# Performance work log

Hardware: AMD Instinct MI355X
Metric: run time of the kernel (lower is better)

The kernel has to match this reference:

```python
import jax, jax.numpy as jnp
import numpy as np

POS_FREQ = 6
DIR_FREQ = 4
HIDDEN = 128
N = 1048576


def pos_encode(x, num_freq):
    # x: (..., D) -> (..., D * 2 * num_freq); per-dim layout [sin(f0..fL-1), cos(f0..fL-1)]
    freqs = 2.0 ** jnp.arange(num_freq, dtype=x.dtype)
    xf = x[..., None] * freqs * jnp.pi  # (..., D, L)
    enc = jnp.concatenate([jnp.sin(xf), jnp.cos(xf)], axis=-1)  # (..., D, 2L)
    return enc.reshape(*x.shape[:-1], x.shape[-1] * 2 * num_freq)


def _linear_params(key, fan_in, fan_out):
    kw, kb = jax.random.split(key)
    bound = 1.0 / np.sqrt(fan_in)
    w = jax.random.uniform(kw, (fan_in, fan_out), jnp.float32, -bound, bound)
    b = jax.random.uniform(kb, (fan_out,), jnp.float32, -bound, bound)
    return w, b


def setup_inputs() -> dict:
    key = jax.random.key(0)
    ks = jax.random.split(key, 12)
    pos_in = 3 * 2 * POS_FREQ   # 36
    dir_in = 3 * 2 * DIR_FREQ   # 24
    positions = jax.random.uniform(ks[0], (N, 3), jnp.float32)
    directions = jax.random.normal(ks[1], (N, 3), jnp.float32)
    directions = directions / jnp.linalg.norm(directions, axis=-1, keepdims=True)
    g1_w, g1_b = _linear_params(ks[2], pos_in, HIDDEN)
    g2_w, g2_b = _linear_params(ks[3], HIDDEN, HIDDEN)
    g3_w, g3_b = _linear_params(ks[4], HIDDEN, HIDDEN)
    g4_w, g4_b = _linear_params(ks[5], HIDDEN, HIDDEN)
    d_w, d_b = _linear_params(ks[6], HIDDEN, 1)
    f_w, f_b = _linear_params(ks[7], HIDDEN, HIDDEN)
    c1_w, c1_b = _linear_params(ks[8], HIDDEN + dir_in, HIDDEN // 2)
    c2_w, c2_b = _linear_params(ks[9], HIDDEN // 2, 3)
    return {
        "positions": positions, "directions": directions,
        "g1_w": g1_w, "g1_b": g1_b, "g2_w": g2_w, "g2_b": g2_b,
        "g3_w": g3_w, "g3_b": g3_b, "g4_w": g4_w, "g4_b": g4_b,
        "d_w": d_w, "d_b": d_b, "f_w": f_w, "f_b": f_b,
        "c1_w": c1_w, "c1_b": c1_b, "c2_w": c2_w, "c2_b": c2_b,
    }


def reference(positions, directions,
              g1_w, g1_b, g2_w, g2_b, g3_w, g3_b, g4_w, g4_b,
              d_w, d_b, f_w, f_b, c1_w, c1_b, c2_w, c2_b):
    pos_enc = pos_encode(positions, POS_FREQ)   # (N, 36)
    dir_enc = pos_encode(directions, DIR_FREQ)  # (N, 24)
    h = jax.nn.relu(pos_enc @ g1_w + g1_b)
    h = jax.nn.relu(h @ g2_w + g2_b)
    h = jax.nn.relu(h @ g3_w + g3_b)
    geo_feat = jax.nn.relu(h @ g4_w + g4_b)     # (N, 128)
    density = jax.nn.softplus(geo_feat @ d_w + d_b)  # (N, 1)
    feature = geo_feat @ f_w + f_b              # (N, 128)
    color_in = jnp.concatenate([feature, dir_enc], axis=-1)  # (N, 152)
    c = jax.nn.relu(color_in @ c1_w + c1_b)
    rgb = jax.nn.sigmoid(c @ c2_w + c2_b)       # (N, 3)
    return rgb, density.squeeze(-1)
```

## Files before the change

kernel.cpp:

```cpp
#include <hip/hip_runtime.h>


typedef _Float16 half8 __attribute__((ext_vector_type(8)));
typedef _Float16 half2v __attribute__((ext_vector_type(2)));
typedef float f32x4 __attribute__((ext_vector_type(4)));

typedef __attribute__((address_space(1))) const unsigned int GU32;
typedef __attribute__((address_space(3))) unsigned int LU32;

#define MFMA16(A,B,C) __builtin_amdgcn_mfma_f32_16x16x32_f16(A,B,C,0,0,0)

#define G1A 0
#define G1B 4096
#define G2A 8192
#define G2B 16384
#define G3A 24576
#define G3B 32768
#define G4A 40960
#define G4B 49152
#define DCH 57344
#define FAC 59392
#define FBC 67584
#define C1C 75776
#define C2C 88064
#define IMG_HALVES 90112

__device__ __forceinline__ int permk(int s){
  int ks = s >> 5, gg = (s >> 3) & 3, jj = s & 7;
  return (2*ks + (jj >> 2))*16 + gg*4 + (jj & 3);
}

__global__ void prep(const float* __restrict__ g1w, const float* __restrict__ g2w,
                     const float* __restrict__ g3w, const float* __restrict__ g4w,
                     const float* __restrict__ dw,  const float* __restrict__ fw,
                     const float* __restrict__ c1w, const float* __restrict__ c2w,
                     _Float16* __restrict__ img) {
  int i = blockIdx.x*256 + threadIdx.x;
  if (i >= IMG_HALVES) return;
  float v; int o_loc, s, krowb, cb;
  if (i < G2A) {
    cb = (i < G1B) ? G1A : G1B; int obase = (i < G1B) ? 0 : 64;
    int r = i - cb; o_loc = r >> 6; s = r & 63; krowb = 128;
    v = (s < 36) ? g1w[s*128 + obase + o_loc] : 0.f;
  } else if (i < DCH) {
    int r = i - G2A; int ch = r >> 13;
    cb = G2A + ch*8192; int li = r & 8191;
    const float* W = (ch < 2) ? g2w : (ch < 4) ? g3w : g4w;
    int obase = (ch & 1)*64;
    o_loc = li >> 7; s = li & 127; krowb = 256;
    v = W[permk(s)*128 + obase + o_loc];
  } else if (i < FAC) {
    cb = DCH; int r = i - DCH; o_loc = r >> 7; s = r & 127; krowb = 256;
    v = (o_loc == 0) ? dw[permk(s)] : 0.f;
  } else if (i < C1C) {
    cb = (i < FBC) ? FAC : FBC; int obase = (i < FBC) ? 0 : 64;
    int r = i - cb; o_loc = r >> 7; s = r & 127; krowb = 256;
    v = fw[permk(s)*128 + obase + o_loc];
  } else if (i < C2C) {
    cb = C1C; int r = i - C1C; o_loc = r/192; s = r%192; krowb = 384;
    v = (s < 128) ? c1w[permk(s)*64 + o_loc]
      : (s < 152) ? c1w[s*64 + o_loc] : 0.f;
  } else {
    cb = C2C; int r = i - C2C; o_loc = r >> 7; s = r & 127; krowb = 256;
    v = (s < 64 && o_loc < 3) ? c2w[permk(s)*3 + o_loc] : 0.f;
  }
  int byte_in = (o_loc*krowb + 2*s) ^ ((o_loc & 7) << 4);
  *(_Float16*)((char*)img + (size_t)cb*2 + byte_in) = (_Float16)v;
}

__device__ __forceinline__ half8 mk8(uint2 a, uint2 b){
  union { unsigned int u[4]; half8 h; } x;
  x.u[0]=a.x; x.u[1]=a.y; x.u[2]=b.x; x.u[3]=b.y; return x.h;
}
__device__ __forceinline__ half8 mkh8(float a,float b,float c,float d,
                                      float e,float f,float g,float h){
  half8 r; r[0]=(_Float16)a; r[1]=(_Float16)b; r[2]=(_Float16)c; r[3]=(_Float16)d;
  r[4]=(_Float16)e; r[5]=(_Float16)f; r[6]=(_Float16)g; r[7]=(_Float16)h; return r;
}
__device__ __forceinline__ uint2 pack4(float a0,float a1,float a2,float a3,bool relu){
  if (relu){ a0=fmaxf(a0,0.f); a1=fmaxf(a1,0.f); a2=fmaxf(a2,0.f); a3=fmaxf(a3,0.f); }
  union { _Float16 h[4]; uint2 u; } x;
  x.h[0]=(_Float16)a0; x.h[1]=(_Float16)a1; x.h[2]=(_Float16)a2; x.h[3]=(_Float16)a3;
  return x.u;
}

template<int KROWB, int KS, int PKB, bool RELU>
__device__ __forceinline__ void chunk64(const _Float16* __restrict__ buf, int lane,
                                        const float* __restrict__ bias,
                                        const half8 (&bf)[4][5], uint2 (&pk)[8][4]) {
  const int g = lane >> 4, n = lane & 15;
  const int swz = (lane & 7) << 4;
  const char* lb = (const char*)buf + n*KROWB;
#pragma unroll
  for (int og = 0; og < 4; ++og) {
    half8 wf[KS];
#pragma unroll
    for (int ks = 0; ks < KS; ++ks)
      wf[ks] = *(const half8*)(lb + og*16*KROWB + ((ks*64 + g*16) ^ swz));
    f32x4 bv = *(const f32x4*)(bias + og*16 + g*4);
    f32x4 acc[4];
#pragma unroll
    for (int st = 0; st < 4; ++st) acc[st] = bv;
#pragma unroll
    for (int ks = 0; ks < KS; ++ks)
#pragma unroll
      for (int st = 0; st < 4; ++st)
        acc[st] = MFMA16(wf[ks], bf[st][ks], acc[st]);
#pragma unroll
    for (int st = 0; st < 4; ++st)
      pk[PKB+og][st] = pack4(acc[st][0], acc[st][1], acc[st][2], acc[st][3], RELU);
  }
}

#define STAGE(BASE_HALF, BUFSEL, ROUNDS) do{ \
  const char* s_ = (const char*)img + (size_t)(BASE_HALF)*2 + tid*16; \
  char* d_ = (char*)(&wbuf[BUFSEL][0]) + wave*1024; \
  _Pragma("unroll") \
  for (int r_ = 0; r_ < (ROUNDS); ++r_) \
    __builtin_amdgcn_global_load_lds((GU32*)(s_ + (size_t)r_*4096), \
                                     (LU32*)(d_ + r_*4096), 16, 0, 0); \
}while(0)

#define REB4() do{ \
  _Pragma("unroll") \
  for (int st_ = 0; st_ < 4; ++st_){ \
    half8 n0 = mk8(pk[0][st_], pk[1][st_]); \
    half8 n1 = mk8(pk[2][st_], pk[3][st_]); \
    half8 n2 = mk8(pk[4][st_], pk[5][st_]); \
    half8 n3 = mk8(pk[6][st_], pk[7][st_]); \
    bf[st_][0]=n0; bf[st_][1]=n1; bf[st_][2]=n2; bf[st_][3]=n3; \
  } \
}while(0)

__global__ __launch_bounds__(256, 2) void nerf_fused(
    const float* __restrict__ pos, const float* __restrict__ dirs,
    const _Float16* __restrict__ img,
    const float* __restrict__ b1, const float* __restrict__ b2,
    const float* __restrict__ b3, const float* __restrict__ b4,
    const float* __restrict__ bd, const float* __restrict__ bfl,
    const float* __restrict__ bc1, const float* __restrict__ bc2,
    float* __restrict__ out, int N) {
  __shared__ _Float16 wbuf[2][12288];
  const int tid = threadIdx.x, wave = tid >> 6, lane = tid & 63;
  const int g = lane >> 4, n = lane & 15;
  const int pbase = blockIdx.x*256 + wave*64;

  half8 bf[4][5];
  uint2 pk[8][4];
  half8 dirf[4];

  STAGE(G1A, 0, 2);

  const float PI = 3.14159265358979f;
  half8 z = {};
#pragma unroll
  for (int st = 0; st < 4; ++st) {
    int p = pbase + st*16 + n;
    float S[3][6], C[3][6];
    const float* pp = pos + (size_t)p*3;
#pragma unroll
    for (int d = 0; d < 3; ++d) {
      float x = pp[d]*PI;
      float s = __sinf(x), c = __cosf(x);
      S[d][0]=s; C[d][0]=c;
#pragma unroll
      for (int l = 1; l < 6; ++l) {
        float s2 = 2.f*s*c, c2 = c*c - s*s;
        S[d][l]=s2; C[d][l]=c2; s=s2; c=c2;
      }
    }
    half8 e0, e1 = z;
    if (g == 0) {
      e0 = mkh8(S[0][0],S[0][1],S[0][2],S[0][3],S[0][4],S[0][5],C[0][0],C[0][1]);
      e1 = mkh8(C[2][2],C[2][3],C[2][4],C[2][5],0.f,0.f,0.f,0.f);
    } else if (g == 1) {
      e0 = mkh8(C[0][2],C[0][3],C[0][4],C[0][5],S[1][0],S[1][1],S[1][2],S[1][3]);
    } else if (g == 2) {
      e0 = mkh8(S[1][4],S[1][5],C[1][0],C[1][1],C[1][2],C[1][3],C[1][4],C[1][5]);
    } else {
      e0 = mkh8(S[2][0],S[2][1],S[2][2],S[2][3],S[2][4],S[2][5],C[2][0],C[2][1]);
    }
    bf[st][0]=e0; bf[st][1]=e1;
    float dv = (g < 3) ? dirs[(size_t)p*3 + g] : 0.f;
    float xx = dv*PI;
    float s1 = __sinf(xx), c1 = __cosf(xx);
    float sa[4], ca[4]; sa[0]=s1; ca[0]=c1;
#pragma unroll
    for (int l = 1; l < 4; ++l) {
      float s2 = 2.f*s1*c1, c2 = c1*c1 - s1*s1;
      sa[l]=s2; ca[l]=c2; s1=s2; c1=c2;
    }
    dirf[st] = (g < 3) ? mkh8(sa[0],sa[1],sa[2],sa[3],ca[0],ca[1],ca[2],ca[3]) : z;
  }
  __syncthreads();

  STAGE(G1B, 1, 2);  chunk64<128,2,0,true >(wbuf[0], lane, b1,     bf, pk); __syncthreads();
  STAGE(G2A, 0, 4);  chunk64<128,2,4,true >(wbuf[1], lane, b1+64,  bf, pk); __syncthreads();
  REB4();
  STAGE(G2B, 1, 4);  chunk64<256,4,0,true >(wbuf[0], lane, b2,     bf, pk); __syncthreads();
  STAGE(G3A, 0, 4);  chunk64<256,4,4,true >(wbuf[1], lane, b2+64,  bf, pk); __syncthreads();
  REB4();
  STAGE(G3B, 1, 4);  chunk64<256,4,0,true >(wbuf[0], lane, b3,     bf, pk); __syncthreads();
  STAGE(G4A, 0, 4);  chunk64<256,4,4,true >(wbuf[1], lane, b3+64,  bf, pk); __syncthreads();
  REB4();
  STAGE(G4B, 1, 4);  chunk64<256,4,0,true >(wbuf[0], lane, b4,     bf, pk); __syncthreads();
  STAGE(DCH, 0, 1);  chunk64<256,4,4,true >(wbuf[1], lane, b4+64,  bf, pk); __syncthreads();
  REB4();
  STAGE(FAC, 1, 4);
  {
    const char* lb = (const char*)wbuf[0] + n*256;
    const int swz = (lane & 7) << 4;
    half8 wf[4];
#pragma unroll
    for (int ks = 0; ks < 4; ++ks)
      wf[ks] = *(const half8*)(lb + ((ks*64 + g*16) ^ swz));
    f32x4 a[4];
#pragma unroll
    for (int st = 0; st < 4; ++st) a[st] = f32x4{0.f,0.f,0.f,0.f};
#pragma unroll
    for (int ks = 0; ks < 4; ++ks)
#pragma unroll
      for (int st = 0; st < 4; ++st) a[st] = MFMA16(wf[ks], bf[st][ks], a[st]);
    if (g == 0) {
      float d0 = bd[0];
#pragma unroll
      for (int st = 0; st < 4; ++st) {
        float x = a[st][0] + d0;
        out[(size_t)3*N + pbase + st*16 + n] = fmaxf(x,0.f) + log1pf(__expf(-fabsf(x)));
      }
    }
  }
  __syncthreads();
  STAGE(FBC, 0, 4);  chunk64<256,4,0,false>(wbuf[1], lane, bfl,    bf, pk); __syncthreads();
  STAGE(C1C, 1, 6);  chunk64<256,4,4,false>(wbuf[0], lane, bfl+64, bf, pk); __syncthreads();
  REB4();
#pragma unroll
  for (int st = 0; st < 4; ++st) bf[st][4] = dirf[st];
  STAGE(C2C, 0, 1);  chunk64<384,5,0,true >(wbuf[1], lane, bc1,    bf, pk); __syncthreads();
#pragma unroll
  for (int st = 0; st < 4; ++st) {
    half8 n0 = mk8(pk[0][st], pk[1][st]);
    half8 n1 = mk8(pk[2][st], pk[3][st]);
    bf[st][0]=n0; bf[st][1]=n1;
  }
  {
    const char* lb = (const char*)wbuf[0] + n*256;
    const int swz = (lane & 7) << 4;
    half8 wf[2];
#pragma unroll
    for (int ks = 0; ks < 2; ++ks)
      wf[ks] = *(const half8*)(lb + ((ks*64 + g*16) ^ swz));
    f32x4 a[4];
#pragma unroll
    for (int st = 0; st < 4; ++st) a[st] = f32x4{0.f,0.f,0.f,0.f};
#pragma unroll
    for (int ks = 0; ks < 2; ++ks)
#pragma unroll
      for (int st = 0; st < 4; ++st) a[st] = MFMA16(wf[ks], bf[st][ks], a[st]);
    if (g == 0) {
      float c0 = bc2[0], c1v = bc2[1], c2v = bc2[2];
#pragma unroll
      for (int st = 0; st < 4; ++st) {
        size_t p = (size_t)(pbase + st*16 + n);
        out[p*3+0] = 1.f/(1.f + __expf(-(a[st][0] + c0)));
        out[p*3+1] = 1.f/(1.f + __expf(-(a[st][1] + c1v)));
        out[p*3+2] = 1.f/(1.f + __expf(-(a[st][2] + c2v)));
      }
    }
  }
}

extern "C" void kernel_launch(void* const* d_in, const int* in_sizes, int n_in,
                              void* d_out, int out_size, void* d_ws, size_t ws_size,
                              hipStream_t stream) {
  const float* pos = (const float*)d_in[0];
  const float* dirs = (const float*)d_in[1];
  const float* g1w = (const float*)d_in[2];
  const float* g1b = (const float*)d_in[3];
  const float* g2w = (const float*)d_in[4];
  const float* g2b = (const float*)d_in[5];
  const float* g3w = (const float*)d_in[6];
  const float* g3b = (const float*)d_in[7];
  const float* g4w = (const float*)d_in[8];
  const float* g4b = (const float*)d_in[9];
  const float* dw  = (const float*)d_in[10];
  const float* db  = (const float*)d_in[11];
  const float* fw  = (const float*)d_in[12];
  const float* fb  = (const float*)d_in[13];
  const float* c1w = (const float*)d_in[14];
  const float* c1b = (const float*)d_in[15];
  const float* c2w = (const float*)d_in[16];
  const float* c2b = (const float*)d_in[17];

  int N = in_sizes[0] / 3;
  _Float16* img = (_Float16*)d_ws;

  prep<<<(IMG_HALVES + 255)/256, 256, 0, stream>>>(
      g1w, g2w, g3w, g4w, dw, fw, c1w, c2w, img);

  nerf_fused<<<N/256, 256, 0, stream>>>(
      pos, dirs, img, g1b, g2b, g3b, g4b, db, fb, c1b, c2b,
      (float*)d_out, N);
}
```

Baseline: 187.0 us.

## Keep all compacted weights resident in LDS across a persistent 1024-thread block

Compacts the packed fp16 weight image: layer-1 rows trimmed to 40 halves, C1 rows to 160 halves, C2 to 64. The density weights move into C1's padding and are computed with fdot2 plus shuffles instead of a separate MFMA chunk. Each 1024-thread block loads the whole ~160KB image into LDS once, then each wave handles four 64-point tiles with no per-layer staging or barriers. s_setprio is also raised around the MFMA loops. This trades per-layer double-buffered streaming for one up-front load, at the cost of large LDS use (one block per CU) and a serial start before any compute.

```diff
diff --git a/kernel.cpp b/kernel.cpp
--- a/kernel.cpp
+++ b/kernel.cpp
@@ -11,19 +11,18 @@
 #define MFMA16(A,B,C) __builtin_amdgcn_mfma_f32_16x16x32_f16(A,B,C,0,0,0)
 
 #define G1A 0
-#define G1B 4096
-#define G2A 8192
-#define G2B 16384
-#define G3A 24576
-#define G3B 32768
-#define G4A 40960
-#define G4B 49152
-#define DCH 57344
-#define FAC 59392
-#define FBC 67584
-#define C1C 75776
-#define C2C 88064
-#define IMG_HALVES 90112
+#define G1B 2560
+#define G2A 5120
+#define G2B 13312
+#define G3A 21504
+#define G3B 29696
+#define G4A 37888
+#define G4B 46080
+#define FAC 54272
+#define FBC 62464
+#define C1C 70656
+#define C2C 80896
+#define IMG_HALVES 81920
 
 __device__ __forceinline__ int permk(int s){
   int ks = s >> 5, gg = (s >> 3) & 3, jj = s & 7;
@@ -37,35 +36,37 @@
                      _Float16* __restrict__ img) {
   int i = blockIdx.x*256 + threadIdx.x;
   if (i >= IMG_HALVES) return;
-  float v; int o_loc, s, krowb, cb;
+  float v = 0.f;
+  size_t byteoff;
   if (i < G2A) {
-    cb = (i < G1B) ? G1A : G1B; int obase = (i < G1B) ? 0 : 64;
-    int r = i - cb; o_loc = r >> 6; s = r & 63; krowb = 128;
-    v = (s < 36) ? g1w[s*128 + obase + o_loc] : 0.f;
-  } else if (i < DCH) {
-    int r = i - G2A; int ch = r >> 13;
-    cb = G2A + ch*8192; int li = r & 8191;
-    const float* W = (ch < 2) ? g2w : (ch < 4) ? g3w : g4w;
-    int obase = (ch & 1)*64;
-    o_loc = li >> 7; s = li & 127; krowb = 256;
-    v = W[permk(s)*128 + obase + o_loc];
-  } else if (i < FAC) {
-    cb = DCH; int r = i - DCH; o_loc = r >> 7; s = r & 127; krowb = 256;
-    v = (o_loc == 0) ? dw[permk(s)] : 0.f;
+    int hf = (i < G1B) ? 0 : 1;
+    int r = i - hf*G1B;
+    int o = r / 40, s = r % 40;
+    v = (s < 36) ? g1w[s*128 + hf*64 + o] : 0.f;
+    byteoff = (size_t)i*2;
   } else if (i < C1C) {
-    cb = (i < FBC) ? FAC : FBC; int obase = (i < FBC) ? 0 : 64;
-    int r = i - cb; o_loc = r >> 7; s = r & 127; krowb = 256;
-    v = fw[permk(s)*128 + obase + o_loc];
+    int ci = (i - G2A) >> 13;
+    int r  = (i - G2A) & 8191;
+    int o = r >> 7, s = r & 127;
+    const float* W = (ci < 2) ? g2w : (ci < 4) ? g3w : (ci < 6) ? g4w : fw;
+    int obase = (ci & 1)*64;
+    v = W[permk(s)*128 + obase + o];
+    byteoff = (size_t)(G2A + ci*8192)*2 + o*256 + ((2*s) ^ ((o & 7) << 4));
   } else if (i < C2C) {
-    cb = C1C; int r = i - C1C; o_loc = r/192; s = r%192; krowb = 384;
-    v = (s < 128) ? c1w[permk(s)*64 + o_loc]
-      : (s < 152) ? c1w[s*64 + o_loc] : 0.f;
+    int r = i - C1C;
+    int o = r / 160, s = r % 160;
+    if (s < 128)      v = c1w[permk(s)*64 + o];
+    else if (s < 152) v = c1w[s*64 + o];
+    else if (o < 16)  v = dw[permk(8*o + (s - 152))];
+    else              v = 0.f;
+    byteoff = (size_t)C1C*2 + o*320 + ((2*s) ^ ((o & 3) << 4));
   } else {
-    cb = C2C; int r = i - C2C; o_loc = r >> 7; s = r & 127; krowb = 256;
-    v = (s < 64 && o_loc < 3) ? c2w[permk(s)*3 + o_loc] : 0.f;
+    int r = i - C2C;
+    int o = r >> 6, s = r & 63;
+    v = (o < 3) ? c2w[permk(s)*3 + o] : 0.f;
+    byteoff = (size_t)C2C*2 + o*128 + ((2*s) ^ ((o & 7) << 4));
   }
-  int byte_in = (o_loc*krowb + 2*s) ^ ((o_loc & 7) << 4);
-  *(_Float16*)((char*)img + (size_t)cb*2 + byte_in) = (_Float16)v;
+  *(_Float16*)((char*)img + byteoff) = (_Float16)v;
 }
 
 __device__ __forceinline__ half8 mk8(uint2 a, uint2 b){
@@ -84,12 +85,12 @@
   return x.u;
 }
 
-template<int KROWB, int KS, int PKB, bool RELU>
-__device__ __forceinline__ void chunk64(const _Float16* __restrict__ buf, int lane,
+template<int KROWB, int KS, int PKB, bool RELU, int SWZM>
+__device__ __forceinline__ void chunk64(const _Float16* buf, int lane,
                                         const float* __restrict__ bias,
                                         const half8 (&bf)[4][5], uint2 (&pk)[8][4]) {
   const int g = lane >> 4, n = lane & 15;
-  const int swz = (lane & 7) << 4;
+  const int swz = (n & SWZM) << 4;
   const char* lb = (const char*)buf + n*KROWB;
 #pragma unroll
   for (int og = 0; og < 4; ++og) {
@@ -101,25 +102,18 @@
     f32x4 acc[4];
 #pragma unroll
     for (int st = 0; st < 4; ++st) acc[st] = bv;
+    __builtin_amdgcn_s_setprio(1);
 #pragma unroll
     for (int ks = 0; ks < KS; ++ks)
 #pragma unroll
       for (int st = 0; st < 4; ++st)
         acc[st] = MFMA16(wf[ks], bf[st][ks], acc[st]);
+    __builtin_amdgcn_s_setprio(0);
 #pragma unroll
     for (int st = 0; st < 4; ++st)
       pk[PKB+og][st] = pack4(acc[st][0], acc[st][1], acc[st][2], acc[st][3], RELU);
   }
 }
-
-#define STAGE(BASE_HALF, BUFSEL, ROUNDS) do{ \
-  const char* s_ = (const char*)img + (size_t)(BASE_HALF)*2 + tid*16; \
-  char* d_ = (char*)(&wbuf[BUFSEL][0]) + wave*1024; \
-  _Pragma("unroll") \
-  for (int r_ = 0; r_ < (ROUNDS); ++r_) \
-    __builtin_amdgcn_global_load_lds((GU32*)(s_ + (size_t)r_*4096), \
-                                     (LU32*)(d_ + r_*4096), 16, 0, 0); \
-}while(0)
 
 #define REB4() do{ \
   _Pragma("unroll") \
@@ -132,7 +126,7 @@
   } \
 }while(0)
 
-__global__ __launch_bounds__(256, 2) void nerf_fused(
+__global__ __launch_bounds__(1024, 4) void nerf_fused(
     const float* __restrict__ pos, const float* __restrict__ dirs,
     const _Float16* __restrict__ img,
     const float* __restrict__ b1, const float* __restrict__ b2,
@@ -140,131 +134,154 @@
     const float* __restrict__ bd, const float* __restrict__ bfl,
     const float* __restrict__ bc1, const float* __restrict__ bc2,
     float* __restrict__ out, int N) {
-  __shared__ _Float16 wbuf[2][12288];
+  __shared__ __align__(16) _Float16 W[IMG_HALVES];
   const int tid = threadIdx.x, wave = tid >> 6, lane = tid & 63;
   const int g = lane >> 4, n = lane & 15;
-  const int pbase = blockIdx.x*256 + wave*64;
+
+#pragma unroll
+  for (int r = 0; r < 10; ++r)
+    __builtin_amdgcn_global_load_lds((GU32*)((const char*)img + tid*16 + (size_t)r*16384),
+                                     (LU32*)((char*)&W[0] + tid*16 + r*16384), 16, 0, 0);
+  __syncthreads();
 
   half8 bf[4][5];
   uint2 pk[8][4];
   half8 dirf[4];
-
-  STAGE(G1A, 0, 2);
-
   const float PI = 3.14159265358979f;
   half8 z = {};
-#pragma unroll
-  for (int st = 0; st < 4; ++st) {
-    int p = pbase + st*16 + n;
-    float S[3][6], C[3][6];
-    const float* pp = pos + (size_t)p*3;
-#pragma unroll
-    for (int d = 0; d < 3; ++d) {
-      float x = pp[d]*PI;
-      float s = __sinf(x), c = __cosf(x);
-      S[d][0]=s; C[d][0]=c;
-#pragma unroll
-      for (int l = 1; l < 6; ++l) {
-        float s2 = 2.f*s*c, c2 = c*c - s*s;
-        S[d][l]=s2; C[d][l]=c2; s=s2; c=c2;
-      }
+
+  for (int it = 0; it < 4; ++it) {
+    const int pbase = (blockIdx.x*64 + wave*4 + it)*64;
+
+#pragma unroll
+    for (int st = 0; st < 4; ++st) {
+      int p = pbase + st*16 + n;
+      float S[3][6], C[3][6];
+      const float* pp = pos + (size_t)p*3;
+#pragma unroll
+      for (int d = 0; d < 3; ++d) {
+        float x = pp[d]*PI;
+        float s = __sinf(x), c = __cosf(x);
+        S[d][0]=s; C[d][0]=c;
+#pragma unroll
+        for (int l = 1; l < 6; ++l) {
+          float s2 = 2.f*s*c, c2 = c*c - s*s;
+          S[d][l]=s2; C[d][l]=c2; s=s2; c=c2;
+        }
+      }
+      half8 e0, e1 = z;
+      if (g == 0) {
+        e0 = mkh8(S[0][0],S[0][1],S[0][2],S[0][3],S[0][4],S[0][5],C[0][0],C[0][1]);
+        e1 = mkh8(C[2][2],C[2][3],C[2][4],C[2][5],0.f,0.f,0.f,0.f);
+      } else if (g == 1) {
+        e0 = mkh8(C[0][2],C[0][3],C[0][4],C[0][5],S[1][0],S[1][1],S[1][2],S[1][3]);
+      } else if (g == 2) {
+        e0 = mkh8(S[1][4],S[1][5],C[1][0],C[1][1],C[1][2],C[1][3],C[1][4],C[1][5]);
+      } else {
+        e0 = mkh8(S[2][0],S[2][1],S[2][2],S[2][3],S[2][4],S[2][5],C[2][0],C[2][1]);
+      }
+      bf[st][0]=e0; bf[st][1]=e1;
+      float dv = (g < 3) ? dirs[(size_t)p*3 + g] : 0.f;
+      float xx = dv*PI;
+      float s1 = __sinf(xx), c1 = __cosf(xx);
+      float sa[4], ca[4]; sa[0]=s1; ca[0]=c1;
+#pragma unroll
+      for (int l = 1; l < 4; ++l) {
+        float s2 = 2.f*s1*c1, c2 = c1*c1 - s1*s1;
+        sa[l]=s2; ca[l]=c2; s1=s2; c1=c2;
+      }
+      dirf[st] = (g < 3) ? mkh8(sa[0],sa[1],sa[2],sa[3],ca[0],ca[1],ca[2],ca[3]) : z;
     }
-    half8 e0, e1 = z;
-    if (g == 0) {
-      e0 = mkh8(S[0][0],S[0][1],S[0][2],S[0][3],S[0][4],S[0][5],C[0][0],C[0][1]);
-      e1 = mkh8(C[2][2],C[2][3],C[2][4],C[2][5],0.f,0.f,0.f,0.f);
-    } else if (g == 1) {
-      e0 = mkh8(C[0][2],C[0][3],C[0][4],C[0][5],S[1][0],S[1][1],S[1][2],S[1][3]);
-    } else if (g == 2) {
-      e0 = mkh8(S[1][4],S[1][5],C[1][0],C[1][1],C[1][2],C[1][3],C[1][4],C[1][5]);
-    } else {
-      e0 = mkh8(S[2][0],S[2][1],S[2][2],S[2][3],S[2][4],S[2][5],C[2][0],C[2][1]);
+
+    chunk64< 80,2,0,true ,0>(&W[G1A], lane, b1,     bf, pk);
+    chunk64< 80,2,4,true ,0>(&W[G1B], lane, b1+64,  bf, pk);
+    REB4();
+    chunk64<256,4,0,true ,7>(&W[G2A], lane, b2,     bf, pk);
+    chunk64<256,4,4,true ,7>(&W[G2B], lane, b2+64,  bf, pk);
+    REB4();
+    chunk64<256,4,0,true ,7>(&W[G3A], lane, b3,     bf, pk);
+    chunk64<256,4,4,true ,7>(&W[G3B], lane, b3+64,  bf, pk);
+    REB4();
+    chunk64<256,4,0,true ,7>(&W[G4A], lane, b4,     bf, pk);
+    chunk64<256,4,4,true ,7>(&W[G4B], lane, b4+64,  bf, pk);
+    REB4();
+
+    {
+      half8 dv[4];
+#pragma unroll
+      for (int ks = 0; ks < 4; ++ks) {
+        int o = ks*4 + g;
+        dv[ks] = *(const half8*)((const char*)&W[C1C] + o*320 + (304 ^ ((o & 3) << 4)));
+      }
+      float dsum[4];
+#pragma unroll
+      for (int st = 0; st < 4; ++st) {
+        float a = 0.f;
+#pragma unroll
+        for (int ks = 0; ks < 4; ++ks)
+#pragma unroll
+          for (int q = 0; q < 4; ++q) {
+#if __has_builtin(__builtin_amdgcn_fdot2)
+            half2v xv = {bf[st][ks][2*q], bf[st][ks][2*q+1]};
+            half2v wv = {dv[ks][2*q],     dv[ks][2*q+1]};
+            a = __builtin_amdgcn_fdot2(xv, wv, a, false);
+#else
+            a += (float)bf[st][ks][2*q]   * (float)dv[ks][2*q];
+            a += (float)bf[st][ks][2*q+1] * (float)dv[ks][2*q+1];
+#endif
+          }
+        a += __shfl_xor(a, 16);
+        a += __shfl_xor(a, 32);
+        dsum[st] = a;
+      }
+      if (g == 0) {
+        float d0 = bd[0];
+#pragma unroll
+        for (int st = 0; st < 4; ++st) {
+          float x = dsum[st] + d0;
+          out[(size_t)3*N + pbase + st*16 + n] = fmaxf(x,0.f) + log1pf(__expf(-fabsf(x)));
+        }
+      }
     }
-    bf[st][0]=e0; bf[st][1]=e1;
-    float dv = (g < 3) ? dirs[(size_t)p*3 + g] : 0.f;
-    float xx = dv*PI;
-    float s1 = __sinf(xx), c1 = __cosf(xx);
-    float sa[4], ca[4]; sa[0]=s1; ca[0]=c1;
-#pragma unroll
-    for (int l = 1; l < 4; ++l) {
-      float s2 = 2.f*s1*c1, c2 = c1*c1 - s1*s1;
-      sa[l]=s2; ca[l]=c2; s1=s2; c1=c2;
+
+    chunk64<256,4,0,false,7>(&W[FAC], lane, bfl,    bf, pk);
+    chunk64<256,4,4,false,7>(&W[FBC], lane, bfl+64, bf, pk);
+    REB4();
+#pragma unroll
+    for (int st = 0; st < 4; ++st) bf[st][4] = dirf[st];
+
+    chunk64<320,5,0,true ,3>(&W[C1C], lane, bc1,    bf, pk);
+#pragma unroll
+    for (int st = 0; st < 4; ++st) {
+      bf[st][0] = mk8(pk[0][st], pk[1][st]);
+      bf[st][1] = mk8(pk[2][st], pk[3][st]);
     }
-    dirf[st] = (g < 3) ? mkh8(sa[0],sa[1],sa[2],sa[3],ca[0],ca[1],ca[2],ca[3]) : z;
-  }
-  __syncthreads();
-
-  STAGE(G1B, 1, 2);  chunk64<128,2,0,true >(wbuf[0], lane, b1,     bf, pk); __syncthreads();
-  STAGE(G2A, 0, 4);  chunk64<128,2,4,true >(wbuf[1], lane, b1+64,  bf, pk); __syncthreads();
-  REB4();
-  STAGE(G2B, 1, 4);  chunk64<256,4,0,true >(wbuf[0], lane, b2,     bf, pk); __syncthreads();
-  STAGE(G3A, 0, 4);  chunk64<256,4,4,true >(wbuf[1], lane, b2+64,  bf, pk); __syncthreads();
-  REB4();
-  STAGE(G3B, 1, 4);  chunk64<256,4,0,true >(wbuf[0], lane, b3,     bf, pk); __syncthreads();
-  STAGE(G4A, 0, 4);  chunk64<256,4,4,true >(wbuf[1], lane, b3+64,  bf, pk); __syncthreads();
-  REB4();
-  STAGE(G4B, 1, 4);  chunk64<256,4,0,true >(wbuf[0], lane, b4,     bf, pk); __syncthreads();
-  STAGE(DCH, 0, 1);  chunk64<256,4,4,true >(wbuf[1], lane, b4+64,  bf, pk); __syncthreads();
-  REB4();
-  STAGE(FAC, 1, 4);
-  {
-    const char* lb = (const char*)wbuf[0] + n*256;
-    const int swz = (lane & 7) << 4;
-    half8 wf[4];
-#pragma unroll
-    for (int ks = 0; ks < 4; ++ks)
-      wf[ks] = *(const half8*)(lb + ((ks*64 + g*16) ^ swz));
-    f32x4 a[4];
-#pragma unroll
-    for (int st = 0; st < 4; ++st) a[st] = f32x4{0.f,0.f,0.f,0.f};
-#pragma unroll
-    for (int ks = 0; ks < 4; ++ks)
-#pragma unroll
-      for (int st = 0; st < 4; ++st) a[st] = MFMA16(wf[ks], bf[st][ks], a[st]);
-    if (g == 0) {
-      float d0 = bd[0];
-#pragma unroll
-      for (int st = 0; st < 4; ++st) {
-        float x = a[st][0] + d0;
-        out[(size_t)3*N + pbase + st*16 + n] = fmaxf(x,0.f) + log1pf(__expf(-fabsf(x)));
-      }
-    }
-  }
-  __syncthreads();
-  STAGE(FBC, 0, 4);  chunk64<256,4,0,false>(wbuf[1], lane, bfl,    bf, pk); __syncthreads();
-  STAGE(C1C, 1, 6);  chunk64<256,4,4,false>(wbuf[0], lane, bfl+64, bf, pk); __syncthreads();
-  REB4();
-#pragma unroll
-  for (int st = 0; st < 4; ++st) bf[st][4] = dirf[st];
-  STAGE(C2C, 0, 1);  chunk64<384,5,0,true >(wbuf[1], lane, bc1,    bf, pk); __syncthreads();
-#pragma unroll
-  for (int st = 0; st < 4; ++st) {
-    half8 n0 = mk8(pk[0][st], pk[1][st]);
-    half8 n1 = mk8(pk[2][st], pk[3][st]);
-    bf[st][0]=n0; bf[st][1]=n1;
-  }
-  {
-    const char* lb = (const char*)wbuf[0] + n*256;
-    const int swz = (lane & 7) << 4;
-    half8 wf[2];
-#pragma unroll
-    for (int ks = 0; ks < 2; ++ks)
-      wf[ks] = *(const half8*)(lb + ((ks*64 + g*16) ^ swz));
-    f32x4 a[4];
-#pragma unroll
-    for (int st = 0; st < 4; ++st) a[st] = f32x4{0.f,0.f,0.f,0.f};
-#pragma unroll
-    for (int ks = 0; ks < 2; ++ks)
-#pragma unroll
-      for (int st = 0; st < 4; ++st) a[st] = MFMA16(wf[ks], bf[st][ks], a[st]);
-    if (g == 0) {
-      float c0 = bc2[0], c1v = bc2[1], c2v = bc2[2];
-#pragma unroll
-      for (int st = 0; st < 4; ++st) {
-        size_t p = (size_t)(pbase + st*16 + n);
-        out[p*3+0] = 1.f/(1.f + __expf(-(a[st][0] + c0)));
-        out[p*3+1] = 1.f/(1.f + __expf(-(a[st][1] + c1v)));
-        out[p*3+2] = 1.f/(1.f + __expf(-(a[st][2] + c2v)));
+
+    {
+      const char* lb = (const char*)&W[C2C] + n*128;
+      const int swz = (n & 7) << 4;
+      half8 wf[2];
+#pragma unroll
+      for (int ks = 0; ks < 2; ++ks)
+        wf[ks] = *(const half8*)(lb + ((ks*64 + g*16) ^ swz));
+      f32x4 a[4];
+#pragma unroll
+      for (int st = 0; st < 4; ++st) a[st] = f32x4{0.f,0.f,0.f,0.f};
+      __builtin_amdgcn_s_setprio(1);
+#pragma unroll
+      for (int ks = 0; ks < 2; ++ks)
+#pragma unroll
+        for (int st = 0; st < 4; ++st) a[st] = MFMA16(wf[ks], bf[st][ks], a[st]);
+      __builtin_amdgcn_s_setprio(0);
+      if (g == 0) {
+        float c0 = bc2[0], c1v = bc2[1], c2v = bc2[2];
+#pragma unroll
+        for (int st = 0; st < 4; ++st) {
+          size_t p = (size_t)(pbase + st*16 + n);
+          out[p*3+0] = 1.f/(1.f + __expf(-(a[st][0] + c0)));
+          out[p*3+1] = 1.f/(1.f + __expf(-(a[st][1] + c1v)));
+          out[p*3+2] = 1.f/(1.f + __expf(-(a[st][2] + c2v)));
+        }
       }
     }
   }
@@ -298,7 +315,7 @@
   prep<<<(IMG_HALVES + 255)/256, 256, 0, stream>>>(
       g1w, g2w, g3w, g4w, dw, fw, c1w, c2w, img);
 
-  nerf_fused<<<N/256, 256, 0, stream>>>(
+  nerf_fused<<<N/4096, 1024, 0, stream>>>(
       pos, dirs, img, g1b, g2b, g3b, g4b, db, fb, c1b, c2b,
       (float*)d_out, N);
 }
```

After: 661.1 us. 253% more time.
